# Kernel optimization log

Measured on AMD Instinct MI355X. Metric: run time of the kernel, lower is better.

## Reference

```python
import jax, jax.numpy as jnp
import numpy as np

E = 7          # num experts
K = 1          # top-k
R = 8          # LoRA rank
C = 768        # channels
DEPTHS = [[0, 1, 2, 3], [4, 5], [6]]   # deep2idx
EPS = float(np.finfo(np.float64).eps)  # np.finfo(float).eps in the torch code


def setup_inputs() -> dict:
    key = jax.random.key(0)
    k0, k1, k2, k3 = jax.random.split(key, 4)
    B, N = 8, 2048
    x = jax.random.normal(k0, (B, N, C), jnp.float32)
    w_gate = jax.random.normal(k1, (C, E), jnp.float32) * 0.02
    # Lora_a weight is [r, C] per expert (nn.Linear(in, d).weight); Lora_b is [C, r].
    Wa = jax.random.normal(k2, (3, E, R, C), jnp.float32) * 0.02
    Wb = jax.random.normal(k3, (3, E, C, R), jnp.float32) * 0.02
    return {"x": x, "w_gate": w_gate, "Wa": Wa, "Wb": Wb}


def _cv_squared(v):
    # torch .var() default is unbiased (ddof=1)
    return jnp.var(v, ddof=1) / (jnp.mean(v) ** 2 + 1e-10)


def _gating(xf, w_gate):
    # eval-mode noisy_top_k_gating (no noise): top-k of clean logits, softmax over top-k
    logits = xf @ w_gate                                   # [T, E]
    top_vals, top_idx = jax.lax.top_k(logits, K + 1)        # m = k+1
    gate_vals = jax.nn.softmax(top_vals[:, :K], axis=1)     # [T, K]
    rows = jnp.arange(xf.shape[0])[:, None]
    gates = jnp.zeros_like(logits).at[rows, top_idx[:, :K]].set(gate_vals)
    return gates                                            # [T, E]


def _expert_outputs(xf, Wa_a, Wb_a):
    # All-expert LoRA outputs (dense-masked equivalent of SparseDispatcher):
    # lora_i(x) = (x @ Wa_i^T) @ Wb_i^T  -- rank-8 grouped GEMMs
    h = jnp.einsum('erc,tc->etr', Wa_a, xf)                 # [E, T, R]
    lora = jnp.einsum('edr,etr->etd', Wb_a, h)              # [E, T, C]
    outs = [None] * E
    for j in DEPTHS[0]:
        outs[j] = lora[j]
    prev = DEPTHS[0]
    for lvl in (1, 2):  # hierarchical: own LoRA + mean of previous-level expert outputs
        prev_mean = sum(outs[j] for j in prev) / float(len(prev))
        for i in DEPTHS[lvl]:
            outs[i] = lora[i] + prev_mean
        prev = DEPTHS[lvl]
    return jnp.stack(outs)                                  # [E, T, C]


def reference(x, w_gate, Wa, Wb):
    B, N, Cc = x.shape
    xf = x.reshape(B * N, Cc)                               # token-level gating path
    gates = _gating(xf, w_gate)                             # [T, E]
    importance = gates.sum(0)
    load = (gates > 0).sum(0).astype(jnp.float32)           # _gates_to_load
    loss = _cv_squared(importance) + _cv_squared(load)
    ys = []
    for a in range(3):  # q, k, v adapters
        outs = _expert_outputs(xf, Wa[a], Wb[a])            # [E, T, C]
        # SparseDispatcher.combine: log( index_add( exp(expert_out) * gate ) )
        comb = jnp.einsum('te,etc->tc', gates, jnp.exp(outs))
        comb = jnp.where(comb == 0, EPS, comb)
        ys.append(jnp.log(comb))
    return jnp.stack(ys), loss                              # ([3, T, C], scalar)
```

## Files before the change

kernel.cpp:

```cpp
#include <hip/hip_runtime.h>

#define C_DIM 768


__global__ __launch_bounds__(256) void transpose_w(
    const float* __restrict__ wa, const float* __restrict__ wg,
    const float* __restrict__ wb,
    float4* __restrict__ waT4, float4* __restrict__ wbT4) {
  const int b = blockIdx.x;
  if (b < 144) {
    const int g = b * 256 + threadIdx.x;
    const int o = g % 192, k4 = g / 192;
    float4 v = make_float4(0.f, 0.f, 0.f, 0.f);
    if (o < 168) {
      v = *(const float4*)(wa + (size_t)o * C_DIM + k4 * 4);
    } else if (o < 175) {
      const int e = o - 168;
      v.x = wg[(k4 * 4 + 0) * 7 + e];
      v.y = wg[(k4 * 4 + 1) * 7 + e];
      v.z = wg[(k4 * 4 + 2) * 7 + e];
      v.w = wg[(k4 * 4 + 3) * 7 + e];
    }
    waT4[g] = v;
  } else {
    const int g = (b - 144) * 256 + threadIdx.x;
    const int c4 = g % 192, ak = g / 192;
    const int a = ak / 56, k = ak - a * 56;
    const int e = k >> 3, r = k & 7;
    const float* s = wb + ((size_t)(a * 7 + e) * C_DIM + c4 * 4) * 8 + r;
    wbT4[g] = make_float4(s[0], s[8], s[16], s[24]);
  }
}

__global__ __launch_bounds__(576, 5) void moe_main(
    const float* __restrict__ x, const float4* __restrict__ waT4,
    const float4* __restrict__ wbT4, float* __restrict__ out,
    unsigned int* __restrict__ counts, int T) {
  __shared__ float4 xs4[16 * 192];
  __shared__ float4 hsT4[192 * 4];
  __shared__ int bes[16];

  const int tid = threadIdx.x;
  const int w = tid / 64, lane = tid % 64;
  const int t0 = blockIdx.x * 16;
  float* hs = (float*)hsT4;

  const float4* x4 = (const float4*)x;
  for (int g = tid; g < 3072; g += 576) xs4[g] = x4[(size_t)t0 * 192 + g];
  for (int g = tid; g < 768; g += 576) hsT4[g] = make_float4(0.f, 0.f, 0.f, 0.f);
  __syncthreads();

  const int oi = w / 3, ki = w % 3;
  const int o1 = oi * 64 + lane;
  float acc[16];
  #pragma unroll
  for (int t = 0; t < 16; ++t) acc[t] = 0.f;

  const float4* wa_p = waT4 + (size_t)(ki * 64) * 192 + o1;
  const float4* xk = xs4 + ki * 64;
  float4 wv0 = wa_p[0];
  float4 wv1 = wa_p[192];

  #pragma unroll 2
  for (int s = 0; s < 64; ++s) {
    const float4 wv = (s & 1) ? wv1 : wv0;
    int sn = s + 2; sn = sn > 63 ? 63 : sn;
    if (s & 1) wv1 = wa_p[(size_t)sn * 192];
    else       wv0 = wa_p[(size_t)sn * 192];
    #pragma unroll
    for (int t = 0; t < 16; ++t) {
      const float4 xv = xk[t * 192 + s];
      float v = acc[t];
      v = fmaf(xv.x, wv.x, v);
      v = fmaf(xv.y, wv.y, v);
      v = fmaf(xv.z, wv.z, v);
      v = fmaf(xv.w, wv.w, v);
      acc[t] = v;
    }
  }

  #pragma unroll
  for (int j = 0; j < 16; ++j) {
    const int t = (lane + j) & 15;
    atomicAdd(hs + o1 * 16 + t, acc[t]);
  }
  __syncthreads();

  if (w == 0 && lane < 16) {
    const int t = lane;
    float best = hs[168 * 16 + t];
    int b = 0;
    #pragma unroll
    for (int e = 1; e < 7; ++e) {
      const float lv = hs[(168 + e) * 16 + t];
      if (lv > best) { best = lv; b = e; }
    }
    bes[t] = b;
    atomicAdd(&counts[b], 1u);
  }
  __syncthreads();

  for (int g = tid; g < 168 * 16; g += 576) {
    const int o = g >> 4, t = g & 15;
    const int e = (o % 56) >> 3, b = bes[t];
    float co = (e == b) ? 1.f : 0.f;
    if (b >= 4 && e < 4) co += 0.25f;
    if (b == 6 && (e == 4 || e == 5)) co += 0.5f;
    hs[g] *= co;
  }
  __syncthreads();

  const int a = w / 3, ci = w % 3;
  const float4* wb_p = wbT4 + (size_t)(a * 56) * 192 + ci * 64 + lane;
  const float4* hrow = hsT4 + (size_t)(a * 56) * 4;

  float4 acc2[16];
  #pragma unroll
  for (int t = 0; t < 16; ++t) acc2[t] = make_float4(0.f, 0.f, 0.f, 0.f);

  float4 u0 = wb_p[0];
  float4 u1 = wb_p[192];

  #pragma unroll 2
  for (int k = 0; k < 56; ++k) {
    const float4 u = (k & 1) ? u1 : u0;
    int kn = k + 2; kn = kn > 55 ? 55 : kn;
    if (k & 1) u1 = wb_p[(size_t)kn * 192];
    else       u0 = wb_p[(size_t)kn * 192];
    #pragma unroll
    for (int q = 0; q < 4; ++q) {
      const float4 hq = hrow[k * 4 + q];
      const float hh[4] = {hq.x, hq.y, hq.z, hq.w};
      #pragma unroll
      for (int j = 0; j < 4; ++j) {
        const float s = hh[j];
        float4 A = acc2[q * 4 + j];
        A.x = fmaf(u.x, s, A.x);
        A.y = fmaf(u.y, s, A.y);
        A.z = fmaf(u.z, s, A.z);
        A.w = fmaf(u.w, s, A.w);
        acc2[q * 4 + j] = A;
      }
    }
  }

  float4* out4 = (float4*)out;
  const size_t obase = ((size_t)a * T + t0) * 192 + ci * 64 + lane;
  #pragma unroll
  for (int t = 0; t < 16; ++t) out4[obase + (size_t)t * 192] = acc2[t];
}

__global__ void loss_k(const unsigned int* __restrict__ counts,
                       float* __restrict__ out, int T) {
  if (threadIdx.x == 0) {
    float c[7], mean = 0.f;
    #pragma unroll
    for (int e = 0; e < 7; ++e) { c[e] = (float)counts[e]; mean += c[e]; }
    mean *= (1.f / 7.f);
    float var = 0.f;
    #pragma unroll
    for (int e = 0; e < 7; ++e) { const float d = c[e] - mean; var += d * d; }
    var *= (1.f / 6.f);
    out[(size_t)3 * T * C_DIM] = 2.f * (var / (mean * mean + 1e-10f));
  }
}

extern "C" void kernel_launch(void* const* d_in, const int* in_sizes, int n_in,
                              void* d_out, int out_size, void* d_ws, size_t ws_size,
                              hipStream_t stream) {
  const float* x  = (const float*)d_in[0];
  const float* wg = (const float*)d_in[1];
  const float* Wa = (const float*)d_in[2];
  const float* Wb = (const float*)d_in[3];
  float* out = (float*)d_out;

  unsigned int* counts = (unsigned int*)d_ws;
  float4* waT4 = (float4*)((char*)d_ws + 1024);
  float4* wbT4 = (float4*)((char*)d_ws + 590848);

  const int T = in_sizes[0] / C_DIM;

  hipMemsetAsync(counts, 0, 8 * sizeof(unsigned int), stream);
  transpose_w<<<dim3(270), dim3(256), 0, stream>>>(Wa, wg, Wb, waT4, wbT4);
  moe_main<<<dim3(T / 16), dim3(576), 0, stream>>>(x, waT4, wbT4, out, counts, T);
  loss_k<<<dim3(1), dim3(64), 0, stream>>>(counts, out, T);
}
```

Baseline: 466.6 us.

## Split fused MoE LoRA kernel into separate down-projection and up-projection kernels

Splits the single fused kernel into two. stage1 handles the gating and rank-8 down-projection for 8 tokens per 256-thread block. It writes the coefficient-scaled intermediate h to a transposed workspace buffer. stage2 computes the up-projection over a 2D grid of (token tiles of 32, adapter) and reads h back from global memory. The split is meant to raise occupancy and parallelism compared with the heavy 576-thread fused block, at the cost of an extra global round-trip for h and an additional kernel launch.

```diff
diff --git a/kernel.cpp b/kernel.cpp
--- a/kernel.cpp
+++ b/kernel.cpp
@@ -32,67 +32,77 @@
   }
 }
 
-__global__ __launch_bounds__(576, 5) void moe_main(
+__global__ __launch_bounds__(256, 2) void stage1(
     const float* __restrict__ x, const float4* __restrict__ waT4,
-    const float4* __restrict__ wbT4, float* __restrict__ out,
-    unsigned int* __restrict__ counts, int T) {
-  __shared__ float4 xs4[16 * 192];
-  __shared__ float4 hsT4[192 * 4];
-  __shared__ int bes[16];
+    float* __restrict__ hT, unsigned int* __restrict__ counts, int T) {
+  __shared__ float4 xw[4][384];
+  __shared__ float hs[192 * 9];
+  __shared__ int bes[8];
 
   const int tid = threadIdx.x;
-  const int w = tid / 64, lane = tid % 64;
-  const int t0 = blockIdx.x * 16;
-  float* hs = (float*)hsT4;
+  const int w = tid >> 6, lane = tid & 63;
+  const int t0 = blockIdx.x * 8;
+
+  for (int g = tid; g < 192 * 9; g += 256) hs[g] = 0.f;
 
   const float4* x4 = (const float4*)x;
-  for (int g = tid; g < 3072; g += 576) xs4[g] = x4[(size_t)t0 * 192 + g];
-  for (int g = tid; g < 768; g += 576) hsT4[g] = make_float4(0.f, 0.f, 0.f, 0.f);
-  __syncthreads();
-
-  const int oi = w / 3, ki = w % 3;
-  const int o1 = oi * 64 + lane;
-  float acc[16];
-  #pragma unroll
-  for (int t = 0; t < 16; ++t) acc[t] = 0.f;
-
-  const float4* wa_p = waT4 + (size_t)(ki * 64) * 192 + o1;
-  const float4* xk = xs4 + ki * 64;
-  float4 wv0 = wa_p[0];
-  float4 wv1 = wa_p[192];
+  #pragma unroll
+  for (int j = 0; j < 6; ++j) {
+    const int f = lane + 64 * j;
+    const int t = f / 48, s = f - t * 48;
+    xw[w][f] = x4[(size_t)(t0 + t) * 192 + w * 48 + s];
+  }
+  __syncthreads();
+
+  float acc[8][3];
+  #pragma unroll
+  for (int t = 0; t < 8; ++t)
+    #pragma unroll
+    for (int m = 0; m < 3; ++m) acc[t][m] = 0.f;
+
+  const float4* wa_p = waT4 + (size_t)(w * 48) * 192 + lane;
+  float4 wv[2][3];
+  #pragma unroll
+  for (int m = 0; m < 3; ++m) wv[0][m] = wa_p[64 * m];
+  #pragma unroll
+  for (int m = 0; m < 3; ++m) wv[1][m] = wa_p[192 + 64 * m];
 
   #pragma unroll 2
-  for (int s = 0; s < 64; ++s) {
-    const float4 wv = (s & 1) ? wv1 : wv0;
-    int sn = s + 2; sn = sn > 63 ? 63 : sn;
-    if (s & 1) wv1 = wa_p[(size_t)sn * 192];
-    else       wv0 = wa_p[(size_t)sn * 192];
-    #pragma unroll
-    for (int t = 0; t < 16; ++t) {
-      const float4 xv = xk[t * 192 + s];
-      float v = acc[t];
-      v = fmaf(xv.x, wv.x, v);
-      v = fmaf(xv.y, wv.y, v);
-      v = fmaf(xv.z, wv.z, v);
-      v = fmaf(xv.w, wv.w, v);
-      acc[t] = v;
-    }
-  }
-
-  #pragma unroll
-  for (int j = 0; j < 16; ++j) {
-    const int t = (lane + j) & 15;
-    atomicAdd(hs + o1 * 16 + t, acc[t]);
-  }
-  __syncthreads();
-
-  if (w == 0 && lane < 16) {
-    const int t = lane;
-    float best = hs[168 * 16 + t];
+  for (int s = 0; s < 48; ++s) {
+    const int p = s & 1;
+    #pragma unroll
+    for (int t = 0; t < 8; ++t) {
+      const float4 xv = xw[w][t * 48 + s];
+      #pragma unroll
+      for (int m = 0; m < 3; ++m) {
+        float v = acc[t][m];
+        v = fmaf(xv.x, wv[p][m].x, v);
+        v = fmaf(xv.y, wv[p][m].y, v);
+        v = fmaf(xv.z, wv[p][m].z, v);
+        v = fmaf(xv.w, wv[p][m].w, v);
+        acc[t][m] = v;
+      }
+    }
+    int sn = s + 2; sn = sn > 47 ? 47 : sn;
+    #pragma unroll
+    for (int m = 0; m < 3; ++m) wv[p][m] = wa_p[(size_t)sn * 192 + 64 * m];
+  }
+
+  #pragma unroll
+  for (int m = 0; m < 3; ++m) {
+    const int o = lane + 64 * m;
+    #pragma unroll
+    for (int t = 0; t < 8; ++t) atomicAdd(&hs[o * 9 + t], acc[t][m]);
+  }
+  __syncthreads();
+
+  if (tid < 8) {
+    const int t = tid;
+    float best = hs[168 * 9 + t];
     int b = 0;
     #pragma unroll
     for (int e = 1; e < 7; ++e) {
-      const float lv = hs[(168 + e) * 16 + t];
+      const float lv = hs[(168 + e) * 9 + t];
       if (lv > best) { best = lv; b = e; }
     }
     bes[t] = b;
@@ -100,54 +110,70 @@
   }
   __syncthreads();
 
-  for (int g = tid; g < 168 * 16; g += 576) {
-    const int o = g >> 4, t = g & 15;
+  for (int g = tid; g < 168 * 8; g += 256) {
+    const int o = g >> 3, t = g & 7;
     const int e = (o % 56) >> 3, b = bes[t];
     float co = (e == b) ? 1.f : 0.f;
     if (b >= 4 && e < 4) co += 0.25f;
     if (b == 6 && (e == 4 || e == 5)) co += 0.5f;
-    hs[g] *= co;
-  }
-  __syncthreads();
-
-  const int a = w / 3, ci = w % 3;
-  const float4* wb_p = wbT4 + (size_t)(a * 56) * 192 + ci * 64 + lane;
-  const float4* hrow = hsT4 + (size_t)(a * 56) * 4;
-
-  float4 acc2[16];
-  #pragma unroll
-  for (int t = 0; t < 16; ++t) acc2[t] = make_float4(0.f, 0.f, 0.f, 0.f);
-
-  float4 u0 = wb_p[0];
-  float4 u1 = wb_p[192];
-
-  #pragma unroll 2
-  for (int k = 0; k < 56; ++k) {
-    const float4 u = (k & 1) ? u1 : u0;
-    int kn = k + 2; kn = kn > 55 ? 55 : kn;
-    if (k & 1) u1 = wb_p[(size_t)kn * 192];
-    else       u0 = wb_p[(size_t)kn * 192];
-    #pragma unroll
-    for (int q = 0; q < 4; ++q) {
-      const float4 hq = hrow[k * 4 + q];
-      const float hh[4] = {hq.x, hq.y, hq.z, hq.w};
+    hT[(size_t)o * T + t0 + t] = hs[o * 9 + t] * co;
+  }
+}
+
+__global__ __launch_bounds__(256, 2) void stage2(
+    const float* __restrict__ hT, const float4* __restrict__ wbT4,
+    float* __restrict__ out, int T) {
+  __shared__ float hl[56][32];
+
+  const int tid = threadIdx.x;
+  const int w = tid >> 6, lane = tid & 63;
+  const int a = blockIdx.y;
+  const int t0 = blockIdx.x * 32;
+  const int tb = w * 8;
+
+  for (int idx = tid; idx < 448; idx += 256) {
+    const int k = idx >> 3, t4 = idx & 7;
+    *(float4*)&hl[k][t4 * 4] =
+        *(const float4*)&hT[(size_t)(a * 56 + k) * T + t0 + t4 * 4];
+  }
+  __syncthreads();
+
+  const float4* wb_l = wbT4 + (size_t)(a * 56) * 192 + lane;
+  float4* out4 = (float4*)out;
+
+  #pragma unroll 1
+  for (int cc = 0; cc < 3; ++cc) {
+    const float4* wp = wb_l + cc * 64;
+    float4 acc[8];
+    #pragma unroll
+    for (int t = 0; t < 8; ++t) acc[t] = make_float4(0.f, 0.f, 0.f, 0.f);
+
+    float4 u0 = wp[0];
+    float4 u1 = wp[192];
+
+    #pragma unroll 4
+    for (int k = 0; k < 56; ++k) {
+      const float4 u = (k & 1) ? u1 : u0;
+      int kn = k + 2; kn = kn > 55 ? 55 : kn;
+      const float4 un = wp[(size_t)kn * 192];
+      const float4 h0 = *(const float4*)&hl[k][tb];
+      const float4 h1 = *(const float4*)&hl[k][tb + 4];
+      const float hv[8] = {h0.x, h0.y, h0.z, h0.w, h1.x, h1.y, h1.z, h1.w};
       #pragma unroll
-      for (int j = 0; j < 4; ++j) {
-        const float s = hh[j];
-        float4 A = acc2[q * 4 + j];
-        A.x = fmaf(u.x, s, A.x);
-        A.y = fmaf(u.y, s, A.y);
-        A.z = fmaf(u.z, s, A.z);
-        A.w = fmaf(u.w, s, A.w);
-        acc2[q * 4 + j] = A;
+      for (int t = 0; t < 8; ++t) {
+        const float s = hv[t];
+        acc[t].x = fmaf(u.x, s, acc[t].x);
+        acc[t].y = fmaf(u.y, s, acc[t].y);
+        acc[t].z = fmaf(u.z, s, acc[t].z);
+        acc[t].w = fmaf(u.w, s, acc[t].w);
       }
-    }
-  }
-
-  float4* out4 = (float4*)out;
-  const size_t obase = ((size_t)a * T + t0) * 192 + ci * 64 + lane;
-  #pragma unroll
-  for (int t = 0; t < 16; ++t) out4[obase + (size_t)t * 192] = acc2[t];
+      if (k & 1) u1 = un; else u0 = un;
+    }
+
+    #pragma unroll
+    for (int t = 0; t < 8; ++t)
+      out4[((size_t)a * T + t0 + tb + t) * 192 + cc * 64 + lane] = acc[t];
+  }
 }
 
 __global__ void loss_k(const unsigned int* __restrict__ counts,
@@ -177,11 +203,13 @@
   unsigned int* counts = (unsigned int*)d_ws;
   float4* waT4 = (float4*)((char*)d_ws + 1024);
   float4* wbT4 = (float4*)((char*)d_ws + 590848);
+  float* hT    = (float*)((char*)d_ws + 1110016);
 
   const int T = in_sizes[0] / C_DIM;
 
   hipMemsetAsync(counts, 0, 8 * sizeof(unsigned int), stream);
   transpose_w<<<dim3(270), dim3(256), 0, stream>>>(Wa, wg, Wb, waT4, wbT4);
-  moe_main<<<dim3(T / 16), dim3(576), 0, stream>>>(x, waT4, wbT4, out, counts, T);
+  stage1<<<dim3(T / 8), dim3(256), 0, stream>>>(x, waT4, hT, counts, T);
+  stage2<<<dim3(T / 32, 3), dim3(256), 0, stream>>>(hT, wbT4, out, T);
   loss_k<<<dim3(1), dim3(64), 0, stream>>>(counts, out, T);
 }
```

Measured after the change: 393.3 us. 1.19x faster.
